# Kernel optimization log

Measured on AMD Instinct MI355X. Metric: run time of the kernel, lower is better.

## Reference

```python
import jax, jax.numpy as jnp
import numpy as np

N_NODES = 50000
N_EDGES = 800000
D = 128
HEADS = 1
N_LAYERS = 3
NEG_SLOPE = 0.2


def setup_inputs() -> dict:
    key = jax.random.key(0)
    ks = jax.random.split(key, 8)
    x = jax.random.normal(ks[0], (N_NODES, D), dtype=jnp.float32)
    edge_index = jax.random.randint(ks[1], (2, N_EDGES), 0, N_NODES, dtype=jnp.int64)
    # Per-layer GATConv params (heads=1): lin [D, H*D], att_src/att_dst [H, D], bias [H*D]
    s = 1.0 / np.sqrt(D)
    W = jax.random.normal(ks[2], (N_LAYERS, D, HEADS * D), dtype=jnp.float32) * s
    att_src = jax.random.normal(ks[3], (N_LAYERS, HEADS, D), dtype=jnp.float32) * s
    att_dst = jax.random.normal(ks[4], (N_LAYERS, HEADS, D), dtype=jnp.float32) * s
    bias = jnp.zeros((N_LAYERS, HEADS * D), dtype=jnp.float32)
    return {"x": x, "edge_index": edge_index, "W": W, "att_src": att_src,
            "att_dst": att_dst, "bias": bias}


def _gat_conv(x, src, dst, W, a_src, a_dst, b):
    # x: [N, D] -> xp: [N, H, C]
    N = x.shape[0]
    xp = (x @ W).reshape(N, HEADS, D)
    alpha_s = jnp.sum(xp * a_src, axis=-1)  # [N, H]
    alpha_d = jnp.sum(xp * a_dst, axis=-1)  # [N, H]
    # per-edge attention logits (message j=src -> i=dst)
    e = alpha_s[src] + alpha_d[dst]                       # [E, H]
    e = jnp.where(e > 0, e, NEG_SLOPE * e)                # leaky_relu(0.2)
    # segment softmax over destination node
    m = jax.ops.segment_max(e, dst, num_segments=N)       # [N, H]
    ex = jnp.exp(e - m[dst])
    denom = jax.ops.segment_sum(ex, dst, num_segments=N)  # [N, H]
    coef = ex / (denom[dst] + 1e-16)                      # [E, H]
    # scatter-aggregate messages
    out = jax.ops.segment_sum(xp[src] * coef[:, :, None], dst, num_segments=N)  # [N, H, C]
    return out.reshape(N, HEADS * D) + b


def reference(x, edge_index, W, att_src, att_dst, bias):
    N = x.shape[0]
    # GATConv default add_self_loops=True: append (i, i) for every node
    loops = jnp.arange(N, dtype=edge_index.dtype)
    src = jnp.concatenate([edge_index[0], loops])
    dst = jnp.concatenate([edge_index[1], loops])
    h = x
    for l in range(N_LAYERS):
        # dropout omitted for deterministic reference (eval-mode semantics)
        h = _gat_conv(h, src, dst, W[l], att_src[l], att_dst[l], bias[l])
        if l < N_LAYERS - 1:
            h = jax.nn.gelu(h)
    return h
```

## Files before the change

### kernel.cpp

```cpp
#include <hip/hip_runtime.h>
#include <hip/hip_bf16.h>
#include <hip/hip_fp16.h>

#define NN    50000
#define NE    800000
#define ETOT  (NE + NN)
#define D     128
#define NB    ((NN + 255) / 256)

typedef _Float16 f16x8 __attribute__((ext_vector_type(8)));
typedef float    f32x4 __attribute__((ext_vector_type(4)));

__device__ __forceinline__ float gelu_fast(float x) {
    float x2 = x * x;
    float z2 = x * fmaf(x2, 0.07135483f, 1.5957691f);
    float e  = __expf(z2);
    return x - __fdividef(x, e + 1.0f);
}


__global__ void count_k(const int* __restrict__ dstarr, int* __restrict__ counts,
                        int* __restrict__ rank) {
    int e = blockIdx.x * blockDim.x + threadIdx.x;
    if (e >= ETOT) return;
    int d = (e < NE) ? dstarr[e] : (e - NE);
    rank[e] = atomicAdd(&counts[d], 1);
}

__global__ void scan1_k(const int* __restrict__ counts, int* __restrict__ blk_sums) {
    __shared__ int sm[4];
    int i = blockIdx.x * 256 + threadIdx.x;
    int v = (i < NN) ? counts[i] : 0;
    #pragma unroll
    for (int o = 32; o; o >>= 1) v += __shfl_xor(v, o);
    if ((threadIdx.x & 63) == 0) sm[threadIdx.x >> 6] = v;
    __syncthreads();
    if (threadIdx.x == 0) blk_sums[blockIdx.x] = sm[0] + sm[1] + sm[2] + sm[3];
}

__global__ void scan2_k(const int* __restrict__ blk_sums, int* __restrict__ blk_offs,
                        int* __restrict__ row_ptr) {
    if (threadIdx.x == 0 && blockIdx.x == 0) {
        int acc = 0;
        for (int b = 0; b < NB; ++b) { blk_offs[b] = acc; acc += blk_sums[b]; }
        row_ptr[NN] = acc;
    }
}

__global__ void scan3_k(const int* __restrict__ counts, const int* __restrict__ blk_offs,
                        int* __restrict__ row_ptr) {
    __shared__ int s[256];
    int t = threadIdx.x;
    int i = blockIdx.x * 256 + t;
    int v = (i < NN) ? counts[i] : 0;
    s[t] = v;
    __syncthreads();
    for (int off = 1; off < 256; off <<= 1) {
        int x = (t >= off) ? s[t - off] : 0;
        __syncthreads();
        s[t] += x;
        __syncthreads();
    }
    int excl = s[t] - v + blk_offs[blockIdx.x];
    if (i < NN) row_ptr[i] = excl;
}

__global__ void scatter2_k(const int* __restrict__ srcarr, const int* __restrict__ dstarr,
                           const int* __restrict__ rank, const int* __restrict__ row_ptr,
                           int* __restrict__ srcs) {
    int e = blockIdx.x * blockDim.x + threadIdx.x;
    if (e >= ETOT) return;
    int d, s;
    if (e < NE) { d = dstarr[e]; s = srcarr[e]; }
    else        { d = e - NE;    s = e - NE; }
    srcs[row_ptr[d] + rank[e]] = s;
}


__global__ void wasd_k(const float* __restrict__ W, const float* __restrict__ asrc,
                       const float* __restrict__ adst, float* __restrict__ wasd) {
    int l = blockIdx.x;
    int t = threadIdx.x;
    int k = t & 127, which = t >> 7;
    const float* wr = W + (size_t)l * D * D + (size_t)k * D;
    const float* av = (which ? adst : asrc) + (size_t)l * D;
    float s = 0.f;
    #pragma unroll 4
    for (int c = 0; c < D; ++c) s += wr[c] * av[c];
    wasd[l * 256 + which * 128 + k] = s;
}


__global__ void wt_k(const float* __restrict__ W, __half* __restrict__ WT) {
    int l = blockIdx.y;
    int i = blockIdx.x * 256 + threadIdx.x;
    int k = i >> 7, c = i & 127;
    WT[(size_t)l * 16384 + (size_t)c * 128 + k] =
        __float2half_rn(W[(size_t)l * 16384 + (size_t)k * 128 + c]);
}


__global__ __launch_bounds__(256) void xcvt_k(
        const float* __restrict__ x, const float* __restrict__ wasd0,
        __half* __restrict__ xh, float* __restrict__ alpha_s, float* __restrict__ alpha_d) {
    int n = (blockIdx.x * blockDim.x + threadIdx.x) >> 6;
    if (n >= NN) return;
    int lane = threadIdx.x & 63;
    float2 v = ((const float2*)(x + (size_t)n * D))[lane];
    ((__half2*)(xh + (size_t)n * D))[lane] = __floats2half2_rn(v.x, v.y);
    float ps = v.x * wasd0[2 * lane] + v.y * wasd0[2 * lane + 1];
    float pd = v.x * wasd0[128 + 2 * lane] + v.y * wasd0[128 + 2 * lane + 1];
    #pragma unroll
    for (int o = 32; o; o >>= 1) {
        ps += __shfl_xor(ps, o);
        pd += __shfl_xor(pd, o);
    }
    if (lane == 0) { alpha_s[n] = ps; alpha_d[n] = pd; }
}


__global__ __launch_bounds__(256) void gemm_mfma_k(
        const __half* __restrict__ TH, const __half* __restrict__ WT,
        __half* __restrict__ XP) {
    __shared__ __half Bs[D * D];
    int t = threadIdx.x;
    #pragma unroll
    for (int it = 0; it < 8; ++it) {
        int b = it * 4096 + t * 16;
        int c = b >> 8;
        int swz = b ^ ((c & 7) << 4);
        *(uint4*)((char*)Bs + swz) = *(const uint4*)((const char*)WT + b);
    }
    __syncthreads();

    int w = t >> 6, lane = t & 63;
    int r0 = (blockIdx.x >> 1) * 256 + w * 64;
    int c0 = (blockIdx.x & 1) * 64;
    int lr = lane & 15, lg = lane >> 4;

    f32x4 acc[4][4];
    #pragma unroll
    for (int i = 0; i < 4; ++i)
        #pragma unroll
        for (int j = 0; j < 4; ++j)
            acc[i][j] = (f32x4){0.f, 0.f, 0.f, 0.f};

    const char* abase = (const char*)TH;
    #pragma unroll
    for (int ks = 0; ks < 4; ++ks) {
        f16x8 bf[4];
        #pragma unroll
        for (int ct = 0; ct < 4; ++ct) {
            int c  = c0 + ct * 16 + lr;
            int kb = ks * 64 + lg * 16;
            int addr = c * 256 + (kb ^ ((c & 7) << 4));
            bf[ct] = *(const f16x8*)((const char*)Bs + addr);
        }
        #pragma unroll
        for (int rt = 0; rt < 4; ++rt) {
            int row = r0 + rt * 16 + lr;
            int rc  = row < NN ? row : NN - 1;
            f16x8 af = *(const f16x8*)(abase + (size_t)rc * 256 + ks * 64 + lg * 16);
            #pragma unroll
            for (int ct = 0; ct < 4; ++ct)
                acc[rt][ct] = __builtin_amdgcn_mfma_f32_16x16x32_f16(
                                  af, bf[ct], acc[rt][ct], 0, 0, 0);
        }
    }

    #pragma unroll
    for (int rt = 0; rt < 4; ++rt) {
        #pragma unroll
        for (int q = 0; q < 4; ++q) {
            int row = r0 + rt * 16 + lg * 4 + q;
            if (row < NN) {
                #pragma unroll
                for (int ct = 0; ct < 4; ++ct) {
                    int col = c0 + ct * 16 + lr;
                    XP[(size_t)row * D + col] = __float2half_rn(acc[rt][ct][q]);
                }
            }
        }
    }
}


template <int OUT32, int GELU, int HAS_NEXT>
__global__ __launch_bounds__(256) void agg_u_k(
        const int* __restrict__ row_ptr, const int* __restrict__ srcs,
        const float* __restrict__ alpha_s, const float* __restrict__ alpha_d,
        const __half* __restrict__ XPH, const float* __restrict__ bias,
        const float* __restrict__ wn,
        void* __restrict__ outp, float* __restrict__ as_nx, float* __restrict__ ad_nx) {
    __shared__ float xch[4][128];
    int wv = threadIdx.x >> 6;
    int n = (blockIdx.x * blockDim.x + threadIdx.x) >> 6;
    int lane = threadIdx.x & 63;
    int beg = row_ptr[n], end = row_ptr[n + 1], deg = end - beg;
    float ad = alpha_d[n];
    int qw = lane >> 4, q = lane & 15;

    float2 fin;

    if (deg <= 64) {
        int sreg = 0;
        float e = -3.4e38f;
        if (lane < deg) {
            sreg = srcs[beg + lane];
            float v = alpha_s[sreg] + ad;
            e = v > 0.f ? v : 0.2f * v;
        }
        float m = e;
        #pragma unroll
        for (int o = 32; o; o >>= 1) m = fmaxf(m, __shfl_xor(m, o));
        float w = (lane < deg) ? __expf(e - m) : 0.f;
        float denom = w;
        #pragma unroll
        for (int o = 32; o; o >>= 1) denom += __shfl_xor(denom, o);

        float acc[8] = {0,0,0,0,0,0,0,0};
        int dgr = (deg + 3) & ~3;
        const char* xb = (const char*)XPH;
        int qb = q << 4;
        int j = 0;
        #define GATHER1(JOFF)                                                    \
            {                                                                    \
                int ee = j + (JOFF) + qw;                                        \
                int   ss = __shfl(sreg, ee); float ww = __shfl(w, ee);           \
                uint4 uu = *(const uint4*)(xb + ((ss << 8) + qb));               \
                union { uint4 u; __half2 h[4]; } U; U.u = uu;                    \
                float2 f0 = __half22float2(U.h[0]);                              \
                float2 f1 = __half22float2(U.h[1]);                              \
                float2 f2 = __half22float2(U.h[2]);                              \
                float2 f3 = __half22float2(U.h[3]);                              \
                acc[0] += ww*f0.x; acc[1] += ww*f0.y;                            \
                acc[2] += ww*f1.x; acc[3] += ww*f1.y;                            \
                acc[4] += ww*f2.x; acc[5] += ww*f2.y;                            \
                acc[6] += ww*f3.x; acc[7] += ww*f3.y;                            \
            }
        for (; j + 16 <= dgr; j += 16) {
            GATHER1(0) GATHER1(4) GATHER1(8) GATHER1(12)
        }
        for (; j < dgr; j += 4) {
            GATHER1(0)
        }
        #undef GATHER1
        #pragma unroll
        for (int f = 0; f < 8; ++f) {
            acc[f] += __shfl_xor(acc[f], 16);
            acc[f] += __shfl_xor(acc[f], 32);
        }
        if (lane < 16) {
            float4* p = (float4*)&xch[wv][q * 8];
            p[0] = make_float4(acc[0], acc[1], acc[2], acc[3]);
            p[1] = make_float4(acc[4], acc[5], acc[6], acc[7]);
        }
        __asm__ volatile("s_waitcnt lgkmcnt(0)" ::: "memory");
        float2 a2 = *(const float2*)&xch[wv][2 * lane];
        float inv = 1.f / (denom + 1e-16f);
        fin.x = a2.x * inv;
        fin.y = a2.y * inv;
    } else {
        float m = -3.4e38f;
        for (int i = beg + lane; i < end; i += 64) {
            int s = srcs[i];
            float v = alpha_s[s] + ad; v = v > 0.f ? v : 0.2f * v;
            m = fmaxf(m, v);
        }
        #pragma unroll
        for (int o = 32; o; o >>= 1) m = fmaxf(m, __shfl_xor(m, o));
        float denom = 0.f;
        for (int i = beg + lane; i < end; i += 64) {
            int s = srcs[i];
            float v = alpha_s[s] + ad; v = v > 0.f ? v : 0.2f * v;
            denom += __expf(v - m);
        }
        #pragma unroll
        for (int o = 32; o; o >>= 1) denom += __shfl_xor(denom, o);
        float2 acc = {0.f, 0.f};
        for (int i = beg; i < end; ++i) {
            int s = srcs[i];
            float v = alpha_s[s] + ad; v = v > 0.f ? v : 0.2f * v;
            float wgt = __expf(v - m);
            union { unsigned int x; __half2 h; } U;
            U.x = ((const unsigned int*)(XPH + (size_t)s * D))[lane];
            float2 f = __half22float2(U.h);
            acc.x += wgt * f.x; acc.y += wgt * f.y;
        }
        float inv = 1.f / (denom + 1e-16f);
        fin.x = acc.x * inv;
        fin.y = acc.y * inv;
    }

    float2 b2 = ((const float2*)bias)[lane];
    fin.x += b2.x;
    fin.y += b2.y;
    if (GELU) { fin.x = gelu_fast(fin.x); fin.y = gelu_fast(fin.y); }

    if (OUT32) {
        ((float2*)((float*)outp + (size_t)n * D))[lane] = fin;
    } else {
        ((__half2*)((__half*)outp + (size_t)n * D))[lane] = __floats2half2_rn(fin.x, fin.y);
    }

    if (HAS_NEXT) {
        float2 ws2 = ((const float2*)wn)[lane];
        float2 wd2 = ((const float2*)(wn + 128))[lane];
        float ps = fin.x * ws2.x + fin.y * ws2.y;
        float pd = fin.x * wd2.x + fin.y * wd2.y;
        #pragma unroll
        for (int o = 32; o; o >>= 1) {
            ps += __shfl_xor(ps, o);
            pd += __shfl_xor(pd, o);
        }
        if (lane == 0) { as_nx[n] = ps; ad_nx[n] = pd; }
    }
}


extern "C" void kernel_launch(void* const* d_in, const int* in_sizes, int n_in,
                              void* d_out, int out_size, void* d_ws, size_t ws_size,
                              hipStream_t stream) {
    const float* x    = (const float*)d_in[0];
    const int*   ei   = (const int*)d_in[1];
    const float* W    = (const float*)d_in[2];
    const float* asrc = (const float*)d_in[3];
    const float* adst = (const float*)d_in[4];
    const float* bias = (const float*)d_in[5];
    float* out = (float*)d_out;

    const int* src_arr = ei;
    const int* dst_arr = ei + NE;

    char* ws = (char*)d_ws;
    size_t off = 0;
    auto alloc = [&](size_t bytes) { char* p = ws + off; off += (bytes + 255) & ~(size_t)255; return p; };
    __half* th_a    = (__half*)alloc((size_t)NN * D * sizeof(__half));
    __half* th_b    = (__half*)alloc((size_t)NN * D * sizeof(__half));
    __half* xph     = (__half*)alloc((size_t)NN * D * sizeof(__half));
    __half* wt      = (__half*)alloc((size_t)3 * D * D * sizeof(__half));
    float*  as_a    = (float*)alloc(NN * sizeof(float));
    float*  ad_a    = (float*)alloc(NN * sizeof(float));
    float*  as_b    = (float*)alloc(NN * sizeof(float));
    float*  ad_b    = (float*)alloc(NN * sizeof(float));
    float*  wasd    = (float*)alloc(3 * 256 * sizeof(float));
    int* counts    = (int*)alloc(NN * sizeof(int));
    int* row_ptr   = (int*)alloc((NN + 1) * sizeof(int));
    int* rank      = (int*)alloc((size_t)ETOT * sizeof(int));
    int* blk_sums  = (int*)alloc(NB * sizeof(int));
    int* blk_offs  = (int*)alloc(NB * sizeof(int));
    int* srcs      = (int*)alloc((size_t)ETOT * sizeof(int));
    (void)ws_size; (void)in_sizes; (void)n_in; (void)out_size;

    hipMemsetAsync(counts, 0, NN * sizeof(int), stream);
    int eb = (ETOT + 255) / 256;
    count_k<<<eb, 256, 0, stream>>>(dst_arr, counts, rank);
    scan1_k<<<NB, 256, 0, stream>>>(counts, blk_sums);
    scan2_k<<<1, 64, 0, stream>>>(blk_sums, blk_offs, row_ptr);
    scan3_k<<<NB, 256, 0, stream>>>(counts, blk_offs, row_ptr);
    scatter2_k<<<eb, 256, 0, stream>>>(src_arr, dst_arr, rank, row_ptr, srcs);

    wasd_k<<<3, 256, 0, stream>>>(W, asrc, adst, wasd);
    wt_k<<<dim3(64, 3), 256, 0, stream>>>(W, wt);
    xcvt_k<<<NN / 4, 256, 0, stream>>>(x, wasd, th_a, as_a, ad_a);

    int gb = 2 * ((NN + 255) / 256);
    int ab = NN / 4;

    gemm_mfma_k<<<gb, 256, 0, stream>>>(th_a, wt, xph);
    agg_u_k<0, 1, 1><<<ab, 256, 0, stream>>>(row_ptr, srcs, as_a, ad_a, xph,
                                             bias, wasd + 256, th_b, as_b, ad_b);
    gemm_mfma_k<<<gb, 256, 0, stream>>>(th_b, wt + 16384, xph);
    agg_u_k<0, 1, 1><<<ab, 256, 0, stream>>>(row_ptr, srcs, as_b, ad_b, xph,
                                             bias + D, wasd + 512, th_a, as_a, ad_a);
    gemm_mfma_k<<<gb, 256, 0, stream>>>(th_a, wt + 32768, xph);
    agg_u_k<1, 0, 0><<<ab, 256, 0, stream>>>(row_ptr, srcs, as_a, ad_a, xph,
                                             bias + 2 * D, nullptr, out, nullptr, nullptr);
}
```

Before: 228.4 us.

## Split projected features into column halves with XCD-aware aggregation, fuse alpha into GEMM

The projected feature matrix is now stored as two 64-column halves. Aggregation launches twice as many blocks, and each wave gathers only one half. Block indices are remapped so that each half is handled by a fixed group of XCDs, which aims to keep each 6.4MB half resident in that group's L2. The attention logits alpha_s/alpha_d are now computed inside the GEMM from the fp16 input rows, not in the aggregation epilogue. This costs redundant softmax-logit work per half and lower fp16 precision for the alpha dot products.

```diff
diff --git a/kernel.cpp b/kernel.cpp
--- a/kernel.cpp
+++ b/kernel.cpp
@@ -101,27 +101,17 @@
 
 
 __global__ __launch_bounds__(256) void xcvt_k(
-        const float* __restrict__ x, const float* __restrict__ wasd0,
-        __half* __restrict__ xh, float* __restrict__ alpha_s, float* __restrict__ alpha_d) {
-    int n = (blockIdx.x * blockDim.x + threadIdx.x) >> 6;
-    if (n >= NN) return;
-    int lane = threadIdx.x & 63;
-    float2 v = ((const float2*)(x + (size_t)n * D))[lane];
-    ((__half2*)(xh + (size_t)n * D))[lane] = __floats2half2_rn(v.x, v.y);
-    float ps = v.x * wasd0[2 * lane] + v.y * wasd0[2 * lane + 1];
-    float pd = v.x * wasd0[128 + 2 * lane] + v.y * wasd0[128 + 2 * lane + 1];
-    #pragma unroll
-    for (int o = 32; o; o >>= 1) {
-        ps += __shfl_xor(ps, o);
-        pd += __shfl_xor(pd, o);
-    }
-    if (lane == 0) { alpha_s[n] = ps; alpha_d[n] = pd; }
+        const float* __restrict__ x, __half* __restrict__ xh) {
+    int i = blockIdx.x * 256 + threadIdx.x;
+    float2 v = ((const float2*)x)[i];
+    ((__half2*)xh)[i] = __floats2half2_rn(v.x, v.y);
 }
 
 
 __global__ __launch_bounds__(256) void gemm_mfma_k(
         const __half* __restrict__ TH, const __half* __restrict__ WT,
-        __half* __restrict__ XP) {
+        const float* __restrict__ wasd,
+        __half* __restrict__ XPH, float* __restrict__ alpha_s, float* __restrict__ alpha_d) {
     __shared__ __half Bs[D * D];
     int t = threadIdx.x;
     #pragma unroll
@@ -137,6 +127,7 @@
     int r0 = (blockIdx.x >> 1) * 256 + w * 64;
     int c0 = (blockIdx.x & 1) * 64;
     int lr = lane & 15, lg = lane >> 4;
+    bool doalpha = (blockIdx.x & 1) == 0;
 
     f32x4 acc[4][4];
     #pragma unroll
@@ -144,6 +135,8 @@
         #pragma unroll
         for (int j = 0; j < 4; ++j)
             acc[i][j] = (f32x4){0.f, 0.f, 0.f, 0.f};
+
+    float ps[4] = {0, 0, 0, 0}, pd[4] = {0, 0, 0, 0};
 
     const char* abase = (const char*)TH;
     #pragma unroll
@@ -156,11 +149,25 @@
             int addr = c * 256 + (kb ^ ((c & 7) << 4));
             bf[ct] = *(const f16x8*)((const char*)Bs + addr);
         }
+        float4 s0, s1, d0, d1;
+        if (doalpha) {
+            const float* wsp = wasd + ks * 32 + lg * 8;
+            s0 = *(const float4*)(wsp);       s1 = *(const float4*)(wsp + 4);
+            d0 = *(const float4*)(wsp + 128); d1 = *(const float4*)(wsp + 132);
+        }
         #pragma unroll
         for (int rt = 0; rt < 4; ++rt) {
             int row = r0 + rt * 16 + lr;
             int rc  = row < NN ? row : NN - 1;
             f16x8 af = *(const f16x8*)(abase + (size_t)rc * 256 + ks * 64 + lg * 16);
+            if (doalpha) {
+                float a0 = (float)af[0], a1 = (float)af[1], a2 = (float)af[2], a3 = (float)af[3];
+                float a4 = (float)af[4], a5 = (float)af[5], a6 = (float)af[6], a7 = (float)af[7];
+                ps[rt] += a0*s0.x + a1*s0.y + a2*s0.z + a3*s0.w
+                        + a4*s1.x + a5*s1.y + a6*s1.z + a7*s1.w;
+                pd[rt] += a0*d0.x + a1*d0.y + a2*d0.z + a3*d0.w
+                        + a4*d1.x + a5*d1.y + a6*d1.z + a7*d1.w;
+            }
             #pragma unroll
             for (int ct = 0; ct < 4; ++ct)
                 acc[rt][ct] = __builtin_amdgcn_mfma_f32_16x16x32_f16(
@@ -168,6 +175,7 @@
         }
     }
 
+    __half* xpt = XPH + (size_t)(c0 >> 6) * NN * 64;
     #pragma unroll
     for (int rt = 0; rt < 4; ++rt) {
         #pragma unroll
@@ -176,31 +184,44 @@
             if (row < NN) {
                 #pragma unroll
                 for (int ct = 0; ct < 4; ++ct) {
-                    int col = c0 + ct * 16 + lr;
-                    XP[(size_t)row * D + col] = __float2half_rn(acc[rt][ct][q]);
+                    int colh = ct * 16 + lr;
+                    xpt[(size_t)row * 64 + colh] = __float2half_rn(acc[rt][ct][q]);
                 }
             }
         }
     }
-}
-
-
-template <int OUT32, int GELU, int HAS_NEXT>
-__global__ __launch_bounds__(256) void agg_u_k(
+
+    if (doalpha) {
+        #pragma unroll
+        for (int rt = 0; rt < 4; ++rt) {
+            float p = ps[rt], dq = pd[rt];
+            p  += __shfl_xor(p, 16);  p  += __shfl_xor(p, 32);
+            dq += __shfl_xor(dq, 16); dq += __shfl_xor(dq, 32);
+            int row = r0 + rt * 16 + lr;
+            if (lane < 16 && row < NN) { alpha_s[row] = p; alpha_d[row] = dq; }
+        }
+    }
+}
+
+
+template <int OUT32, int GELU>
+__global__ __launch_bounds__(256) void agg_h_k(
         const int* __restrict__ row_ptr, const int* __restrict__ srcs,
         const float* __restrict__ alpha_s, const float* __restrict__ alpha_d,
         const __half* __restrict__ XPH, const float* __restrict__ bias,
-        const float* __restrict__ wn,
-        void* __restrict__ outp, float* __restrict__ as_nx, float* __restrict__ ad_nx) {
-    __shared__ float xch[4][128];
-    int wv = threadIdx.x >> 6;
-    int n = (blockIdx.x * blockDim.x + threadIdx.x) >> 6;
-    int lane = threadIdx.x & 63;
+        void* __restrict__ outp) {
+    __shared__ float xch[4][64];
+    int b = blockIdx.x;
+    int xcd  = b & 7;
+    int half = xcd >> 2;
+    int lblk = (b >> 3) * 4 + (xcd & 3);
+    int wv = threadIdx.x >> 6, lane = threadIdx.x & 63;
+    int n = lblk * 4 + wv;
     int beg = row_ptr[n], end = row_ptr[n + 1], deg = end - beg;
     float ad = alpha_d[n];
-    int qw = lane >> 4, q = lane & 15;
-
-    float2 fin;
+    const __half* tab = XPH + (size_t)half * NN * 64;
+    const char* tb = (const char*)tab;
+    float fin;
 
     if (deg <= 64) {
         int sreg = 0;
@@ -218,16 +239,15 @@
         #pragma unroll
         for (int o = 32; o; o >>= 1) denom += __shfl_xor(denom, o);
 
-        float acc[8] = {0,0,0,0,0,0,0,0};
-        int dgr = (deg + 3) & ~3;
-        const char* xb = (const char*)XPH;
-        int qb = q << 4;
+        int og = lane >> 3, qb = (lane & 7) << 4;
+        float acc[8] = {0, 0, 0, 0, 0, 0, 0, 0};
+        int dgr = (deg + 7) & ~7;
         int j = 0;
-        #define GATHER1(JOFF)                                                    \
+        #define GATHER8(JOFF)                                                    \
             {                                                                    \
-                int ee = j + (JOFF) + qw;                                        \
+                int ee = j + (JOFF) + og;                                        \
                 int   ss = __shfl(sreg, ee); float ww = __shfl(w, ee);           \
-                uint4 uu = *(const uint4*)(xb + ((ss << 8) + qb));               \
+                uint4 uu = *(const uint4*)(tb + ((ss << 7) + qb));               \
                 union { uint4 u; __half2 h[4]; } U; U.u = uu;                    \
                 float2 f0 = __half22float2(U.h[0]);                              \
                 float2 f1 = __half22float2(U.h[1]);                              \
@@ -239,27 +259,27 @@
                 acc[6] += ww*f3.x; acc[7] += ww*f3.y;                            \
             }
         for (; j + 16 <= dgr; j += 16) {
-            GATHER1(0) GATHER1(4) GATHER1(8) GATHER1(12)
-        }
-        for (; j < dgr; j += 4) {
-            GATHER1(0)
-        }
-        #undef GATHER1
+            GATHER8(0) GATHER8(8)
+        }
+        for (; j < dgr; j += 8) {
+            GATHER8(0)
+        }
+        #undef GATHER8
         #pragma unroll
         for (int f = 0; f < 8; ++f) {
+            acc[f] += __shfl_xor(acc[f], 8);
             acc[f] += __shfl_xor(acc[f], 16);
             acc[f] += __shfl_xor(acc[f], 32);
         }
-        if (lane < 16) {
-            float4* p = (float4*)&xch[wv][q * 8];
+        if (lane < 8) {
+            float4* p = (float4*)&xch[wv][lane * 8];
             p[0] = make_float4(acc[0], acc[1], acc[2], acc[3]);
             p[1] = make_float4(acc[4], acc[5], acc[6], acc[7]);
         }
         __asm__ volatile("s_waitcnt lgkmcnt(0)" ::: "memory");
-        float2 a2 = *(const float2*)&xch[wv][2 * lane];
+        __builtin_amdgcn_sched_barrier(0);
         float inv = 1.f / (denom + 1e-16f);
-        fin.x = a2.x * inv;
-        fin.y = a2.y * inv;
+        fin = xch[wv][lane] * inv;
     } else {
         float m = -3.4e38f;
         for (int i = beg + lane; i < end; i += 64) {
@@ -277,44 +297,20 @@
         }
         #pragma unroll
         for (int o = 32; o; o >>= 1) denom += __shfl_xor(denom, o);
-        float2 acc = {0.f, 0.f};
+        float acc = 0.f;
         for (int i = beg; i < end; ++i) {
             int s = srcs[i];
             float v = alpha_s[s] + ad; v = v > 0.f ? v : 0.2f * v;
             float wgt = __expf(v - m);
-            union { unsigned int x; __half2 h; } U;
-            U.x = ((const unsigned int*)(XPH + (size_t)s * D))[lane];
-            float2 f = __half22float2(U.h);
-            acc.x += wgt * f.x; acc.y += wgt * f.y;
-        }
-        float inv = 1.f / (denom + 1e-16f);
-        fin.x = acc.x * inv;
-        fin.y = acc.y * inv;
-    }
-
-    float2 b2 = ((const float2*)bias)[lane];
-    fin.x += b2.x;
-    fin.y += b2.y;
-    if (GELU) { fin.x = gelu_fast(fin.x); fin.y = gelu_fast(fin.y); }
-
-    if (OUT32) {
-        ((float2*)((float*)outp + (size_t)n * D))[lane] = fin;
-    } else {
-        ((__half2*)((__half*)outp + (size_t)n * D))[lane] = __floats2half2_rn(fin.x, fin.y);
-    }
-
-    if (HAS_NEXT) {
-        float2 ws2 = ((const float2*)wn)[lane];
-        float2 wd2 = ((const float2*)(wn + 128))[lane];
-        float ps = fin.x * ws2.x + fin.y * ws2.y;
-        float pd = fin.x * wd2.x + fin.y * wd2.y;
-        #pragma unroll
-        for (int o = 32; o; o >>= 1) {
-            ps += __shfl_xor(ps, o);
-            pd += __shfl_xor(pd, o);
-        }
-        if (lane == 0) { as_nx[n] = ps; ad_nx[n] = pd; }
-    }
+            acc += wgt * __half2float(tab[(size_t)s * 64 + lane]);
+        }
+        fin = acc / (denom + 1e-16f);
+    }
+
+    fin += bias[half * 64 + lane];
+    if (GELU) fin = gelu_fast(fin);
+    if (OUT32) ((float*)outp)[(size_t)n * D + half * 64 + lane] = fin;
+    else       ((__half*)outp)[(size_t)n * D + half * 64 + lane] = __float2half_rn(fin);
 }
 
 
@@ -337,12 +333,10 @@
     auto alloc = [&](size_t bytes) { char* p = ws + off; off += (bytes + 255) & ~(size_t)255; return p; };
     __half* th_a    = (__half*)alloc((size_t)NN * D * sizeof(__half));
     __half* th_b    = (__half*)alloc((size_t)NN * D * sizeof(__half));
-    __half* xph     = (__half*)alloc((size_t)NN * D * sizeof(__half));
+    __half* xph     = (__half*)alloc((size_t)2 * NN * 64 * sizeof(__half));
     __half* wt      = (__half*)alloc((size_t)3 * D * D * sizeof(__half));
     float*  as_a    = (float*)alloc(NN * sizeof(float));
     float*  ad_a    = (float*)alloc(NN * sizeof(float));
-    float*  as_b    = (float*)alloc(NN * sizeof(float));
-    float*  ad_b    = (float*)alloc(NN * sizeof(float));
     float*  wasd    = (float*)alloc(3 * 256 * sizeof(float));
     int* counts    = (int*)alloc(NN * sizeof(int));
     int* row_ptr   = (int*)alloc((NN + 1) * sizeof(int));
@@ -362,18 +356,15 @@
 
     wasd_k<<<3, 256, 0, stream>>>(W, asrc, adst, wasd);
     wt_k<<<dim3(64, 3), 256, 0, stream>>>(W, wt);
-    xcvt_k<<<NN / 4, 256, 0, stream>>>(x, wasd, th_a, as_a, ad_a);
+    xcvt_k<<<NN * 64 / 256, 256, 0, stream>>>(x, th_a);
 
     int gb = 2 * ((NN + 255) / 256);
-    int ab = NN / 4;
-
-    gemm_mfma_k<<<gb, 256, 0, stream>>>(th_a, wt, xph);
-    agg_u_k<0, 1, 1><<<ab, 256, 0, stream>>>(row_ptr, srcs, as_a, ad_a, xph,
-                                             bias, wasd + 256, th_b, as_b, ad_b);
-    gemm_mfma_k<<<gb, 256, 0, stream>>>(th_b, wt + 16384, xph);
-    agg_u_k<0, 1, 1><<<ab, 256, 0, stream>>>(row_ptr, srcs, as_b, ad_b, xph,
-                                             bias + D, wasd + 512, th_a, as_a, ad_a);
-    gemm_mfma_k<<<gb, 256, 0, stream>>>(th_a, wt + 32768, xph);
-    agg_u_k<1, 0, 0><<<ab, 256, 0, stream>>>(row_ptr, srcs, as_a, ad_a, xph,
-                                             bias + 2 * D, nullptr, out, nullptr, nullptr);
-}
+    int ab = 2 * (NN / 4);
+
+    gemm_mfma_k<<<gb, 256, 0, stream>>>(th_a, wt, wasd, xph, as_a, ad_a);
+    agg_h_k<0, 1><<<ab, 256, 0, stream>>>(row_ptr, srcs, as_a, ad_a, xph, bias, th_b);
+    gemm_mfma_k<<<gb, 256, 0, stream>>>(th_b, wt + 16384, wasd + 256, xph, as_a, ad_a);
+    agg_h_k<0, 1><<<ab, 256, 0, stream>>>(row_ptr, srcs, as_a, ad_a, xph, bias + D, th_a);
+    gemm_mfma_k<<<gb, 256, 0, stream>>>(th_a, wt + 32768, wasd + 512, xph, as_a, ad_a);
+    agg_h_k<1, 0><<<ab, 256, 0, stream>>>(row_ptr, srcs, as_a, ad_a, xph, bias + 2 * D, out);
+}
```

New measurement: 276.9 us. 21.3% more time.

## Fuse prep kernels, merge scan stages, compute attention logits inside GEMM

Applied to the files above, without the earlier changes.

The edge-count, x conversion, W transpose and wasd precompute move into one multi-role prep kernel, and the serial single-thread block-offset scan is folded into the per-block scan kernel. Each scan block now re-reduces the prefix of block sums itself. The alpha_s/alpha_d dot products move from the aggregation epilogue into the GEMM, using the fp16 A tiles it already loads. The aggregation gather loop is restructured to issue four independent loads before consuming them. These changes cut launch count and the serial scan step, and drop the alpha-buffer ping-pong. In exchange the logits are computed from fp16-rounded inputs, and the scan does redundant prefix work per block.

```diff
diff --git a/kernel.cpp b/kernel.cpp
--- a/kernel.cpp
+++ b/kernel.cpp
@@ -7,6 +7,8 @@
 #define ETOT  (NE + NN)
 #define D     128
 #define NB    ((NN + 255) / 256)
+#define EB    ((ETOT + 255) / 256)
+#define XB    ((NN * 64) / 256)
 
 typedef _Float16 f16x8 __attribute__((ext_vector_type(8)));
 typedef float    f32x4 __attribute__((ext_vector_type(4)));
@@ -19,13 +21,41 @@
 }
 
 
-__global__ void count_k(const int* __restrict__ dstarr, int* __restrict__ counts,
-                        int* __restrict__ rank) {
-    int e = blockIdx.x * blockDim.x + threadIdx.x;
-    if (e >= ETOT) return;
-    int d = (e < NE) ? dstarr[e] : (e - NE);
-    rank[e] = atomicAdd(&counts[d], 1);
-}
+__global__ __launch_bounds__(256) void prep_k(
+        const int* __restrict__ dst_arr, int* __restrict__ counts, int* __restrict__ rank,
+        const float* __restrict__ x, __half* __restrict__ xh,
+        const float* __restrict__ W, __half* __restrict__ WT,
+        const float* __restrict__ asrc, const float* __restrict__ adst,
+        float* __restrict__ wasd) {
+    int b = blockIdx.x, t = threadIdx.x;
+    if (b < EB) {
+        int e = b * 256 + t;
+        if (e < ETOT) {
+            int d = (e < NE) ? dst_arr[e] : (e - NE);
+            rank[e] = atomicAdd(&counts[d], 1);
+        }
+    } else if (b < EB + XB) {
+        int i = (b - EB) * 256 + t;
+        float2 v = ((const float2*)x)[i];
+        ((__half2*)xh)[i] = __floats2half2_rn(v.x, v.y);
+    } else if (b < EB + XB + 192) {
+        int i = (b - EB - XB) * 256 + t;
+        int l = i >> 14, r = i & 16383;
+        int k = r >> 7, c = r & 127;
+        WT[(size_t)l * 16384 + (size_t)c * 128 + k] =
+            __float2half_rn(W[(size_t)l * 16384 + (size_t)k * 128 + c]);
+    } else {
+        int l = b - EB - XB - 192;
+        int k = t & 127, which = t >> 7;
+        const float* wr = W + (size_t)l * 16384 + (size_t)k * 128;
+        const float* av = (which ? adst : asrc) + (size_t)l * 128;
+        float s = 0.f;
+        #pragma unroll 4
+        for (int c = 0; c < 128; ++c) s += wr[c] * av[c];
+        wasd[l * 256 + which * 128 + k] = s;
+    }
+}
+
 
 __global__ void scan1_k(const int* __restrict__ counts, int* __restrict__ blk_sums) {
     __shared__ int sm[4];
@@ -38,20 +68,21 @@
     if (threadIdx.x == 0) blk_sums[blockIdx.x] = sm[0] + sm[1] + sm[2] + sm[3];
 }
 
-__global__ void scan2_k(const int* __restrict__ blk_sums, int* __restrict__ blk_offs,
-                        int* __restrict__ row_ptr) {
-    if (threadIdx.x == 0 && blockIdx.x == 0) {
+__global__ void scan23_k(const int* __restrict__ counts, const int* __restrict__ blk_sums,
+                         int* __restrict__ row_ptr) {
+    __shared__ int s[256];
+    __shared__ int boff_sh;
+    int t = threadIdx.x, bid = blockIdx.x;
+    if (t < 64) {
         int acc = 0;
-        for (int b = 0; b < NB; ++b) { blk_offs[b] = acc; acc += blk_sums[b]; }
-        row_ptr[NN] = acc;
-    }
-}
-
-__global__ void scan3_k(const int* __restrict__ counts, const int* __restrict__ blk_offs,
-                        int* __restrict__ row_ptr) {
-    __shared__ int s[256];
-    int t = threadIdx.x;
-    int i = blockIdx.x * 256 + t;
+        for (int i = t; i < bid; i += 64) acc += blk_sums[i];
+        #pragma unroll
+        for (int o = 32; o; o >>= 1) acc += __shfl_xor(acc, o);
+        if (t == 0) boff_sh = acc;
+    }
+    __syncthreads();
+    int boff = boff_sh;
+    int i = bid * 256 + t;
     int v = (i < NN) ? counts[i] : 0;
     s[t] = v;
     __syncthreads();
@@ -61,8 +92,9 @@
         s[t] += x;
         __syncthreads();
     }
-    int excl = s[t] - v + blk_offs[blockIdx.x];
+    int excl = s[t] - v + boff;
     if (i < NN) row_ptr[i] = excl;
+    if (bid == NB - 1 && t == 255) row_ptr[NN] = s[255] + boff;
 }
 
 __global__ void scatter2_k(const int* __restrict__ srcarr, const int* __restrict__ dstarr,
@@ -77,51 +109,10 @@
 }
 
 
-__global__ void wasd_k(const float* __restrict__ W, const float* __restrict__ asrc,
-                       const float* __restrict__ adst, float* __restrict__ wasd) {
-    int l = blockIdx.x;
-    int t = threadIdx.x;
-    int k = t & 127, which = t >> 7;
-    const float* wr = W + (size_t)l * D * D + (size_t)k * D;
-    const float* av = (which ? adst : asrc) + (size_t)l * D;
-    float s = 0.f;
-    #pragma unroll 4
-    for (int c = 0; c < D; ++c) s += wr[c] * av[c];
-    wasd[l * 256 + which * 128 + k] = s;
-}
-
-
-__global__ void wt_k(const float* __restrict__ W, __half* __restrict__ WT) {
-    int l = blockIdx.y;
-    int i = blockIdx.x * 256 + threadIdx.x;
-    int k = i >> 7, c = i & 127;
-    WT[(size_t)l * 16384 + (size_t)c * 128 + k] =
-        __float2half_rn(W[(size_t)l * 16384 + (size_t)k * 128 + c]);
-}
-
-
-__global__ __launch_bounds__(256) void xcvt_k(
-        const float* __restrict__ x, const float* __restrict__ wasd0,
-        __half* __restrict__ xh, float* __restrict__ alpha_s, float* __restrict__ alpha_d) {
-    int n = (blockIdx.x * blockDim.x + threadIdx.x) >> 6;
-    if (n >= NN) return;
-    int lane = threadIdx.x & 63;
-    float2 v = ((const float2*)(x + (size_t)n * D))[lane];
-    ((__half2*)(xh + (size_t)n * D))[lane] = __floats2half2_rn(v.x, v.y);
-    float ps = v.x * wasd0[2 * lane] + v.y * wasd0[2 * lane + 1];
-    float pd = v.x * wasd0[128 + 2 * lane] + v.y * wasd0[128 + 2 * lane + 1];
-    #pragma unroll
-    for (int o = 32; o; o >>= 1) {
-        ps += __shfl_xor(ps, o);
-        pd += __shfl_xor(pd, o);
-    }
-    if (lane == 0) { alpha_s[n] = ps; alpha_d[n] = pd; }
-}
-
-
 __global__ __launch_bounds__(256) void gemm_mfma_k(
         const __half* __restrict__ TH, const __half* __restrict__ WT,
-        __half* __restrict__ XP) {
+        const float* __restrict__ wasd,
+        __half* __restrict__ XP, float* __restrict__ alpha_s, float* __restrict__ alpha_d) {
     __shared__ __half Bs[D * D];
     int t = threadIdx.x;
     #pragma unroll
@@ -137,6 +128,7 @@
     int r0 = (blockIdx.x >> 1) * 256 + w * 64;
     int c0 = (blockIdx.x & 1) * 64;
     int lr = lane & 15, lg = lane >> 4;
+    bool doalpha = (blockIdx.x & 1) == 0;
 
     f32x4 acc[4][4];
     #pragma unroll
@@ -144,6 +136,8 @@
         #pragma unroll
         for (int j = 0; j < 4; ++j)
             acc[i][j] = (f32x4){0.f, 0.f, 0.f, 0.f};
+
+    float ps[4] = {0, 0, 0, 0}, pd[4] = {0, 0, 0, 0};
 
     const char* abase = (const char*)TH;
     #pragma unroll
@@ -156,11 +150,25 @@
             int addr = c * 256 + (kb ^ ((c & 7) << 4));
             bf[ct] = *(const f16x8*)((const char*)Bs + addr);
         }
+        float4 s0, s1, d0, d1;
+        if (doalpha) {
+            const float* wsp = wasd + ks * 32 + lg * 8;
+            s0 = *(const float4*)(wsp);       s1 = *(const float4*)(wsp + 4);
+            d0 = *(const float4*)(wsp + 128); d1 = *(const float4*)(wsp + 132);
+        }
         #pragma unroll
         for (int rt = 0; rt < 4; ++rt) {
             int row = r0 + rt * 16 + lr;
             int rc  = row < NN ? row : NN - 1;
             f16x8 af = *(const f16x8*)(abase + (size_t)rc * 256 + ks * 64 + lg * 16);
+            if (doalpha) {
+                float a0 = (float)af[0], a1 = (float)af[1], a2 = (float)af[2], a3 = (float)af[3];
+                float a4 = (float)af[4], a5 = (float)af[5], a6 = (float)af[6], a7 = (float)af[7];
+                ps[rt] += a0*s0.x + a1*s0.y + a2*s0.z + a3*s0.w
+                        + a4*s1.x + a5*s1.y + a6*s1.z + a7*s1.w;
+                pd[rt] += a0*d0.x + a1*d0.y + a2*d0.z + a3*d0.w
+                        + a4*d1.x + a5*d1.y + a6*d1.z + a7*d1.w;
+            }
             #pragma unroll
             for (int ct = 0; ct < 4; ++ct)
                 acc[rt][ct] = __builtin_amdgcn_mfma_f32_16x16x32_f16(
@@ -182,16 +190,26 @@
             }
         }
     }
-}
-
-
-template <int OUT32, int GELU, int HAS_NEXT>
+
+    if (doalpha) {
+        #pragma unroll
+        for (int rt = 0; rt < 4; ++rt) {
+            float p = ps[rt], dq = pd[rt];
+            p  += __shfl_xor(p, 16);  p  += __shfl_xor(p, 32);
+            dq += __shfl_xor(dq, 16); dq += __shfl_xor(dq, 32);
+            int row = r0 + rt * 16 + lr;
+            if (lane < 16 && row < NN) { alpha_s[row] = p; alpha_d[row] = dq; }
+        }
+    }
+}
+
+
+template <int OUT32, int GELU>
 __global__ __launch_bounds__(256) void agg_u_k(
         const int* __restrict__ row_ptr, const int* __restrict__ srcs,
         const float* __restrict__ alpha_s, const float* __restrict__ alpha_d,
         const __half* __restrict__ XPH, const float* __restrict__ bias,
-        const float* __restrict__ wn,
-        void* __restrict__ outp, float* __restrict__ as_nx, float* __restrict__ ad_nx) {
+        void* __restrict__ outp) {
     __shared__ float xch[4][128];
     int wv = threadIdx.x >> 6;
     int n = (blockIdx.x * blockDim.x + threadIdx.x) >> 6;
@@ -223,28 +241,36 @@
         const char* xb = (const char*)XPH;
         int qb = q << 4;
         int j = 0;
-        #define GATHER1(JOFF)                                                    \
+        #define PROC(UU, WW)                                                     \
             {                                                                    \
-                int ee = j + (JOFF) + qw;                                        \
-                int   ss = __shfl(sreg, ee); float ww = __shfl(w, ee);           \
-                uint4 uu = *(const uint4*)(xb + ((ss << 8) + qb));               \
-                union { uint4 u; __half2 h[4]; } U; U.u = uu;                    \
+                union { uint4 u; __half2 h[4]; } U; U.u = (UU);                  \
                 float2 f0 = __half22float2(U.h[0]);                              \
                 float2 f1 = __half22float2(U.h[1]);                              \
                 float2 f2 = __half22float2(U.h[2]);                              \
                 float2 f3 = __half22float2(U.h[3]);                              \
-                acc[0] += ww*f0.x; acc[1] += ww*f0.y;                            \
-                acc[2] += ww*f1.x; acc[3] += ww*f1.y;                            \
-                acc[4] += ww*f2.x; acc[5] += ww*f2.y;                            \
-                acc[6] += ww*f3.x; acc[7] += ww*f3.y;                            \
+                acc[0] += (WW)*f0.x; acc[1] += (WW)*f0.y;                        \
+                acc[2] += (WW)*f1.x; acc[3] += (WW)*f1.y;                        \
+                acc[4] += (WW)*f2.x; acc[5] += (WW)*f2.y;                        \
+                acc[6] += (WW)*f3.x; acc[7] += (WW)*f3.y;                        \
             }
         for (; j + 16 <= dgr; j += 16) {
-            GATHER1(0) GATHER1(4) GATHER1(8) GATHER1(12)
+            int   s0 = __shfl(sreg, j + qw);       float w0 = __shfl(w, j + qw);
+            int   s1 = __shfl(sreg, j + 4 + qw);   float w1 = __shfl(w, j + 4 + qw);
+            int   s2 = __shfl(sreg, j + 8 + qw);   float w2 = __shfl(w, j + 8 + qw);
+            int   s3 = __shfl(sreg, j + 12 + qw);  float w3 = __shfl(w, j + 12 + qw);
+            uint4 u0 = *(const uint4*)(xb + ((s0 << 8) + qb));
+            uint4 u1 = *(const uint4*)(xb + ((s1 << 8) + qb));
+            uint4 u2 = *(const uint4*)(xb + ((s2 << 8) + qb));
+            uint4 u3 = *(const uint4*)(xb + ((s3 << 8) + qb));
+            PROC(u0, w0) PROC(u1, w1) PROC(u2, w2) PROC(u3, w3)
         }
         for (; j < dgr; j += 4) {
-            GATHER1(0)
-        }
-        #undef GATHER1
+            int   s0 = __shfl(sreg, j + qw);
+            float w0 = __shfl(w, j + qw);
+            uint4 u0 = *(const uint4*)(xb + ((s0 << 8) + qb));
+            PROC(u0, w0)
+        }
+        #undef PROC
         #pragma unroll
         for (int f = 0; f < 8; ++f) {
             acc[f] += __shfl_xor(acc[f], 16);
@@ -256,6 +282,7 @@
             p[1] = make_float4(acc[4], acc[5], acc[6], acc[7]);
         }
         __asm__ volatile("s_waitcnt lgkmcnt(0)" ::: "memory");
+        __builtin_amdgcn_sched_barrier(0);
         float2 a2 = *(const float2*)&xch[wv][2 * lane];
         float inv = 1.f / (denom + 1e-16f);
         fin.x = a2.x * inv;
@@ -302,19 +329,6 @@
     } else {
         ((__half2*)((__half*)outp + (size_t)n * D))[lane] = __floats2half2_rn(fin.x, fin.y);
     }
-
-    if (HAS_NEXT) {
-        float2 ws2 = ((const float2*)wn)[lane];
-        float2 wd2 = ((const float2*)(wn + 128))[lane];
-        float ps = fin.x * ws2.x + fin.y * ws2.y;
-        float pd = fin.x * wd2.x + fin.y * wd2.y;
-        #pragma unroll
-        for (int o = 32; o; o >>= 1) {
-            ps += __shfl_xor(ps, o);
-            pd += __shfl_xor(pd, o);
-        }
-        if (lane == 0) { as_nx[n] = ps; ad_nx[n] = pd; }
-    }
 }
 
 
@@ -341,39 +355,28 @@
     __half* wt      = (__half*)alloc((size_t)3 * D * D * sizeof(__half));
     float*  as_a    = (float*)alloc(NN * sizeof(float));
     float*  ad_a    = (float*)alloc(NN * sizeof(float));
-    float*  as_b    = (float*)alloc(NN * sizeof(float));
-    float*  ad_b    = (float*)alloc(NN * sizeof(float));
     float*  wasd    = (float*)alloc(3 * 256 * sizeof(float));
     int* counts    = (int*)alloc(NN * sizeof(int));
     int* row_ptr   = (int*)alloc((NN + 1) * sizeof(int));
     int* rank      = (int*)alloc((size_t)ETOT * sizeof(int));
     int* blk_sums  = (int*)alloc(NB * sizeof(int));
-    int* blk_offs  = (int*)alloc(NB * sizeof(int));
     int* srcs      = (int*)alloc((size_t)ETOT * sizeof(int));
     (void)ws_size; (void)in_sizes; (void)n_in; (void)out_size;
 
     hipMemsetAsync(counts, 0, NN * sizeof(int), stream);
-    int eb = (ETOT + 255) / 256;
-    count_k<<<eb, 256, 0, stream>>>(dst_arr, counts, rank);
+    prep_k<<<EB + XB + 192 + 3, 256, 0, stream>>>(dst_arr, counts, rank,
+                                                  x, th_a, W, wt, asrc, adst, wasd);
     scan1_k<<<NB, 256, 0, stream>>>(counts, blk_sums);
-    scan2_k<<<1, 64, 0, stream>>>(blk_sums, blk_offs, row_ptr);
-    scan3_k<<<NB, 256, 0, stream>>>(counts, blk_offs, row_ptr);
-    scatter2_k<<<eb, 256, 0, stream>>>(src_arr, dst_arr, rank, row_ptr, srcs);
-
-    wasd_k<<<3, 256, 0, stream>>>(W, asrc, adst, wasd);
-    wt_k<<<dim3(64, 3), 256, 0, stream>>>(W, wt);
-    xcvt_k<<<NN / 4, 256, 0, stream>>>(x, wasd, th_a, as_a, ad_a);
+    scan23_k<<<NB, 256, 0, stream>>>(counts, blk_sums, row_ptr);
+    scatter2_k<<<EB, 256, 0, stream>>>(src_arr, dst_arr, rank, row_ptr, srcs);
 
     int gb = 2 * ((NN + 255) / 256);
     int ab = NN / 4;
 
-    gemm_mfma_k<<<gb, 256, 0, stream>>>(th_a, wt, xph);
-    agg_u_k<0, 1, 1><<<ab, 256, 0, stream>>>(row_ptr, srcs, as_a, ad_a, xph,
-                                             bias, wasd + 256, th_b, as_b, ad_b);
-    gemm_mfma_k<<<gb, 256, 0, stream>>>(th_b, wt + 16384, xph);
-    agg_u_k<0, 1, 1><<<ab, 256, 0, stream>>>(row_ptr, srcs, as_b, ad_b, xph,
-                                             bias + D, wasd + 512, th_a, as_a, ad_a);
-    gemm_mfma_k<<<gb, 256, 0, stream>>>(th_a, wt + 32768, xph);
-    agg_u_k<1, 0, 0><<<ab, 256, 0, stream>>>(row_ptr, srcs, as_a, ad_a, xph,
-                                             bias + 2 * D, nullptr, out, nullptr, nullptr);
-}
+    gemm_mfma_k<<<gb, 256, 0, stream>>>(th_a, wt, wasd, xph, as_a, ad_a);
+    agg_u_k<0, 1><<<ab, 256, 0, stream>>>(row_ptr, srcs, as_a, ad_a, xph, bias, th_b);
+    gemm_mfma_k<<<gb, 256, 0, stream>>>(th_b, wt + 16384, wasd + 256, xph, as_a, ad_a);
+    agg_u_k<0, 1><<<ab, 256, 0, stream>>>(row_ptr, srcs, as_a, ad_a, xph, bias + D, th_a);
+    gemm_mfma_k<<<gb, 256, 0, stream>>>(th_a, wt + 32768, wasd + 512, xph, as_a, ad_a);
+    agg_u_k<1, 0><<<ab, 256, 0, stream>>>(row_ptr, srcs, as_a, ad_a, xph, bias + 2 * D, out);
+}
```

After: 212.7 us. 1.07x faster.
